# Kernel optimization log

Hardware: AMD Instinct MI355X
Metric: run time of the kernel (lower is better)

Reference implementation:

```python
import jax, jax.numpy as jnp
import numpy as np

# module config
D = 1024      # d_model
H = 16        # n_heads
DK = D // H   # head dim (rotary dim)
HI = 4        # indexer heads
DI = 64       # indexer dim
K = 512       # layer_top_k (adaptive_k fixed to layer default)
B, S = 2, 2048


def setup_inputs() -> dict:
    key = jax.random.key(0)
    ks = jax.random.split(key, 6)
    sc = 0.02
    return {
        "x": jax.random.normal(ks[0], (B, S, D), jnp.float32),
        "w_qkv": jax.random.normal(ks[1], (3 * D, D), jnp.float32) * sc,
        "w_o": jax.random.normal(ks[2], (D, D), jnp.float32) * sc,
        "w_qi": jax.random.normal(ks[3], (HI * DI, D), jnp.float32) * sc,
        "w_ki": jax.random.normal(ks[4], (DI, D), jnp.float32) * sc,
        "w_wi": jax.random.normal(ks[5], (HI, D), jnp.float32) * sc,
    }


def _rope(x):
    # torchtune-style interleaved RoPE; x: [b, s, h, d]
    d = x.shape[-1]
    s = x.shape[1]
    inv = 1.0 / (10000.0 ** (jnp.arange(0, d, 2, dtype=jnp.float32) / d))
    ang = jnp.arange(s, dtype=jnp.float32)[:, None] * inv  # [s, d/2]
    cos = jnp.cos(ang)[None, :, None, :]
    sin = jnp.sin(ang)[None, :, None, :]
    x1, x2 = x[..., ::2], x[..., 1::2]
    return jnp.stack([x1 * cos - x2 * sin, x1 * sin + x2 * cos], axis=-1).reshape(x.shape)


def reference(x, w_qkv, w_o, w_qi, w_ki, w_wi):
    b, s, _ = x.shape
    # QKV projection -> [b, s, 3, H, DK]
    qkv = (x @ w_qkv.T).reshape(b, s, 3, H, DK)
    q, k, v = qkv[:, :, 0], qkv[:, :, 1], qkv[:, :, 2]  # [b, s, h, dk]
    q = _rope(q)
    k = _rope(k)

    # Lightning indexer: I[t,s] = sum_j w[t,j] * relu(q_idx[t,j] . k_idx[s])
    qi = (x @ w_qi.T).reshape(b, s, HI, DI)
    ki = x @ w_ki.T            # [b, s, DI]
    wi = x @ w_wi.T            # [b, s, HI]
    dots = jnp.einsum('bthd,bsd->bths', qi, ki)
    idx_scores = (jax.nn.relu(dots) * wi[:, :, :, None]).sum(axis=2)  # [b, t, s]

    # causal mask then top-k selection -> boolean allow-mask via scatter
    causal = jnp.triu(jnp.ones((s, s), dtype=bool), 1)
    masked_scores = jnp.where(causal[None], -jnp.inf, idx_scores)
    _, top_idx = jax.lax.top_k(masked_scores, K)  # [b, t, K]
    allow = jnp.zeros((b, s, s), dtype=bool).at[
        jnp.arange(b)[:, None, None], jnp.arange(s)[None, :, None], top_idx
    ].set(True)

    # gated sparse attention: SDPA with additive mask (0 where selected, -inf else)
    scores = jnp.einsum('bthd,bshd->bhts', q, k) / jnp.sqrt(jnp.float32(DK))
    scores = jnp.where(allow[:, None], scores, -jnp.inf)
    attn = jax.nn.softmax(scores, axis=-1)
    out = jnp.einsum('bhts,bshd->bthd', attn, v).reshape(b, s, D)
    return out @ w_o.T
```

## Files before the change

### kernel.cpp

```cpp
#include <hip/hip_runtime.h>
#include <hip/hip_bf16.h>
#include <math.h>

namespace {

constexpr int cB = 2, cS = 2048, cD = 1024, cH = 16, cHI = 4, cDI = 64, cK = 512;
constexpr int cNT = cB * cS;
constexpr int QKV_STRIDE = 3 * cD;

typedef __bf16 bf16x8 __attribute__((ext_vector_type(8)));
typedef float f32x4 __attribute__((ext_vector_type(4)));

__device__ __forceinline__ unsigned packbf2(float a, float b)
{
    __hip_bfloat16 ba = __float2bfloat16(a), bb = __float2bfloat16(b);
    return (unsigned)*(unsigned short*)&ba | ((unsigned)*(unsigned short*)&bb << 16);
}

__global__ void pack_bf16(const float* __restrict__ src, __hip_bfloat16* __restrict__ dst, int n)
{
    int i = blockIdx.x * 256 + threadIdx.x;
    if (i < n) dst[i] = __float2bfloat16(src[i]);
}

__global__ __launch_bounds__(256) void mfma_gemm_bt(const __hip_bfloat16* __restrict__ A,
                                                    const __hip_bfloat16* __restrict__ B,
                                                    float* __restrict__ C, int M, int N, int K)
{
    __shared__ unsigned short Als[128][40];
    __shared__ unsigned short Bls[128][40];
    const int tid = threadIdx.x;
    const int m0 = blockIdx.y * 128, n0 = blockIdx.x * 128;
    const int w = tid >> 6, lane = tid & 63;
    const int mw = (w >> 1) * 64, nw = (w & 1) * 64;
    const int lr = lane & 15, quad = lane >> 4;
    const unsigned short* Au = (const unsigned short*)A;
    const unsigned short* Bu = (const unsigned short*)B;
    f32x4 acc[4][4] = {};
    for (int k0 = 0; k0 < K; k0 += 32) {
#pragma unroll
        for (int i = 0; i < 2; i++) {
            int c = tid + i * 256;
            int row = c >> 2, kc = c & 3;
            uint4 av = *(const uint4*)(Au + (size_t)(m0 + row) * K + k0 + kc * 8);
            uint4 bv = *(const uint4*)(Bu + (size_t)(n0 + row) * K + k0 + kc * 8);
            *(uint4*)&Als[row][kc * 8] = av;
            *(uint4*)&Bls[row][kc * 8] = bv;
        }
        __syncthreads();
        bf16x8 af[4], bfr[4];
#pragma unroll
        for (int i = 0; i < 4; i++) af[i] = *(const bf16x8*)&Als[mw + i * 16 + lr][quad * 8];
#pragma unroll
        for (int j = 0; j < 4; j++) bfr[j] = *(const bf16x8*)&Bls[nw + j * 16 + lr][quad * 8];
#pragma unroll
        for (int i = 0; i < 4; i++)
#pragma unroll
            for (int j = 0; j < 4; j++)
                acc[i][j] = __builtin_amdgcn_mfma_f32_16x16x32_bf16(af[i], bfr[j], acc[i][j], 0, 0, 0);
        __syncthreads();
    }
#pragma unroll
    for (int i = 0; i < 4; i++)
#pragma unroll
        for (int j = 0; j < 4; j++)
#pragma unroll
            for (int r = 0; r < 4; r++) {
                int m = m0 + mw + i * 16 + quad * 4 + r;
                int n = n0 + nw + j * 16 + lr;
                C[(size_t)m * N + n] = acc[i][j][r];
            }
}

__global__ __launch_bounds__(256) void gemm_idx(const float* __restrict__ A, const float* __restrict__ w_qi,
                                                const float* __restrict__ w_ki, const float* __restrict__ w_wi,
                                                float* __restrict__ qi, float* __restrict__ ki, float* __restrict__ wi)
{
    __shared__ float As[2][32][68];
    __shared__ float Bs[2][32][68];
    const int tid = threadIdx.x;
    const int m0 = blockIdx.y * 64, n0 = blockIdx.x * 64;
    const int ty = tid >> 4, tx = tid & 15;
    const int r = tid >> 5, kk = tid & 31;
    float aR[8], bR[8];

    auto loadStage = [&](int k0) {
#pragma unroll
        for (int i = 0; i < 8; i++) {
            aR[i] = A[(size_t)(m0 + r + i * 8) * cD + k0 + kk];
            const int nr = n0 + r + i * 8;
            float bv = 0.f;
            if (nr < 256) bv = w_qi[(size_t)nr * cD + k0 + kk];
            else if (nr < 320) bv = w_ki[(size_t)(nr - 256) * cD + k0 + kk];
            else if (nr < 324) bv = w_wi[(size_t)(nr - 320) * cD + k0 + kk];
            bR[i] = bv;
        }
    };
    auto commitStage = [&](int bf) {
#pragma unroll
        for (int i = 0; i < 8; i++) {
            As[bf][kk][r + i * 8] = aR[i];
            Bs[bf][kk][r + i * 8] = bR[i];
        }
    };

    loadStage(0);
    commitStage(0);
    __syncthreads();
    float acc[4][4] = {};
    for (int s = 0; s < 32; s++) {
        const int cb = s & 1;
        if (s < 31) loadStage((s + 1) * 32);
#pragma unroll
        for (int kx = 0; kx < 32; kx++) {
            float a[4], b[4];
#pragma unroll
            for (int i = 0; i < 4; i++) a[i] = As[cb][kx][ty * 4 + i];
#pragma unroll
            for (int j = 0; j < 4; j++) b[j] = Bs[cb][kx][tx * 4 + j];
#pragma unroll
            for (int i = 0; i < 4; i++)
#pragma unroll
                for (int j = 0; j < 4; j++) acc[i][j] = fmaf(a[i], b[j], acc[i][j]);
        }
        if (s < 31) {
            commitStage(cb ^ 1);
            __syncthreads();
        }
    }
#pragma unroll
    for (int i = 0; i < 4; i++) {
        int m = m0 + ty * 4 + i;
#pragma unroll
        for (int j = 0; j < 4; j++) {
            int n = n0 + tx * 4 + j;
            if (n < 256) qi[(size_t)m * 256 + n] = acc[i][j];
            else if (n < 320) ki[(size_t)m * 64 + (n - 256)] = acc[i][j];
            else if (n < 324) wi[(size_t)m * 4 + (n - 320)] = acc[i][j];
        }
    }
}

__global__ void rope_pack(const float* __restrict__ qkv, __hip_bfloat16* __restrict__ qkvb)
{
    const int idx = blockIdx.x * 256 + threadIdx.x;
    const int c = idx & 511, tok = idx >> 9;
    const int i = c & 31;
    const int s = tok & (cS - 1);
    const float inv = powf(10000.f, -(float)(2 * i) / 64.f);
    float sn, cs;
    sincosf((float)s * inv, &sn, &cs);
    const size_t base = (size_t)tok * QKV_STRIDE + (c >> 5) * 64 + 2 * i;
    unsigned* dst = (unsigned*)qkvb;
    float x1 = qkv[base], x2 = qkv[base + 1];
    dst[base >> 1] = packbf2(x1 * cs - x2 * sn, x1 * sn + x2 * cs);
    x1 = qkv[base + cD]; x2 = qkv[base + cD + 1];
    dst[(base + cD) >> 1] = packbf2(x1 * cs - x2 * sn, x1 * sn + x2 * cs);
    dst[(base + 2 * cD) >> 1] = packbf2(qkv[base + 2 * cD], qkv[base + 2 * cD + 1]);
}

__global__ __launch_bounds__(256) void indexer_scores(const float* __restrict__ qi,
                                                      const float* __restrict__ ki,
                                                      const float* __restrict__ wi,
                                                      float* __restrict__ scores)
{
    const int b = blockIdx.z;
    const int t0 = blockIdx.y * 128, s0 = blockIdx.x * 64;
    if (s0 > t0 + 127) return;
    __shared__ float Qs[128][68];
    __shared__ float Ks[64][68];
    const int tid = threadIdx.x;
    const int ty = tid >> 4, tx = tid & 15;
#pragma unroll
    for (int i = 0; i < 4; i++) {
        int c = tid + i * 256;
        int r = c >> 4, cq = c & 15;
        *(float4*)&Ks[r][cq * 4] = *(const float4*)&ki[((size_t)(b * cS + s0 + r)) * cDI + cq * 4];
    }
    float acc[8][4] = {};
    for (int h = 0; h < cHI; h++) {
        __syncthreads();
#pragma unroll
        for (int i = 0; i < 8; i++) {
            int c = tid + i * 256;
            int r = c >> 4, cq = c & 15;
            *(float4*)&Qs[r][cq * 4] =
                *(const float4*)&qi[((size_t)(b * cS + t0 + r)) * (cHI * cDI) + h * cDI + cq * 4];
        }
        __syncthreads();
        float w8[8];
#pragma unroll
        for (int i = 0; i < 8; i++) w8[i] = wi[((size_t)(b * cS + t0 + ty + i * 16)) * cHI + h];
        float dot[8][4] = {};
        for (int d = 0; d < 64; d += 4) {
            float4 a4[8], b4[4];
#pragma unroll
            for (int i = 0; i < 8; i++) a4[i] = *(const float4*)&Qs[ty + i * 16][d];
#pragma unroll
            for (int j = 0; j < 4; j++) b4[j] = *(const float4*)&Ks[tx + j * 16][d];
#pragma unroll
            for (int i = 0; i < 8; i++)
#pragma unroll
                for (int j = 0; j < 4; j++) {
                    dot[i][j] = fmaf(a4[i].x, b4[j].x, dot[i][j]);
                    dot[i][j] = fmaf(a4[i].y, b4[j].y, dot[i][j]);
                    dot[i][j] = fmaf(a4[i].z, b4[j].z, dot[i][j]);
                    dot[i][j] = fmaf(a4[i].w, b4[j].w, dot[i][j]);
                }
        }
#pragma unroll
        for (int i = 0; i < 8; i++)
#pragma unroll
            for (int j = 0; j < 4; j++) acc[i][j] += fmaxf(dot[i][j], 0.f) * w8[i];
    }
#pragma unroll
    for (int i = 0; i < 8; i++) {
        int t = t0 + ty + i * 16;
#pragma unroll
        for (int j = 0; j < 4; j++) {
            int s = s0 + tx + j * 16;
            if (s <= t) scores[((size_t)(b * cS) + t) * cS + s] = acc[i][j];
        }
    }
}

__device__ __forceinline__ unsigned mapf(float f)
{
    unsigned u = __float_as_uint(f);
    if (u == 0x80000000u) u = 0u;
    return (u & 0x80000000u) ? ~u : (u | 0x80000000u);
}

__global__ void topk_select(const float* __restrict__ scores, unsigned* __restrict__ allow_w)
{
    const int row = blockIdx.x;
    const int t = row & (cS - 1);
    const int tid = threadIdx.x;
    unsigned* aw = allow_w + (size_t)row * 64;
    if (t < cK) {
        if (tid < 64) aw[tid] = (tid < 16) ? 0xFFFFFFFFu : 0u;
        return;
    }
    const float* sr = scores + (size_t)row * cS;
    const int n = t + 1;
    __shared__ unsigned ukeys[cS];
    __shared__ int whist[4][16];
    __shared__ unsigned abits[64];
    __shared__ int wsum[4];
    __shared__ unsigned sh_prefix;
    __shared__ int sh_rem, sh_eqbase;
    for (int s = tid; s < n; s += 256) ukeys[s] = mapf(sr[s]);
    if (tid < 64) abits[tid] = 0u;
    if (tid == 0) { sh_prefix = 0u; sh_rem = cK; }
    __syncthreads();
    const int wl = tid >> 6, ln = tid & 63;
    for (int pass = 0; pass < 8; pass++) {
        const int shift = 28 - 4 * pass;
        const unsigned prefix = sh_prefix;
        const unsigned himask = pass ? (0xFFFFFFFFu << (shift + 4)) : 0u;
        unsigned cnt = 0;
        for (int sb = wl * 64; sb < n; sb += 256) {
            const int s = sb + ln;
            const bool active = (s < n) && ((ukeys[s] & himask) == prefix);
            const unsigned d = active ? ((ukeys[s] >> shift) & 15u) : 0u;
            const unsigned long long bA = __ballot(active);
            const unsigned long long b0 = __ballot((d & 1u) != 0u);
            const unsigned long long b1 = __ballot((d & 2u) != 0u);
            const unsigned long long b2 = __ballot((d & 4u) != 0u);
            const unsigned long long b3 = __ballot((d & 8u) != 0u);
            if (ln < 16) {
                unsigned long long mres = bA;
                mres &= (ln & 1) ? b0 : ~b0;
                mres &= (ln & 2) ? b1 : ~b1;
                mres &= (ln & 4) ? b2 : ~b2;
                mres &= (ln & 8) ? b3 : ~b3;
                cnt += (unsigned)__popcll(mres);
            }
        }
        if (ln < 16) whist[wl][ln] = (int)cnt;
        __syncthreads();
        if (tid == 0) {
            int rem = sh_rem, cum = 0, d = 15;
            for (; d > 0; d--) {
                const int hd = whist[0][d] + whist[1][d] + whist[2][d] + whist[3][d];
                if (cum + hd >= rem) break;
                cum += hd;
            }
            sh_prefix = prefix | ((unsigned)d << shift);
            sh_rem = rem - cum;
        }
        __syncthreads();
    }
    const unsigned Tu = sh_prefix;
    const int needEq = sh_rem;
    if (tid == 0) sh_eqbase = 0;
    __syncthreads();
    for (int s0 = 0; s0 < n; s0 += 256) {
        const int s = s0 + tid;
        const bool valid = s < n;
        const unsigned u = valid ? ukeys[s] : 0u;
        const bool gt = valid && (u > Tu);
        const bool eq = valid && (u == Tu);
        const unsigned long long bal = __ballot(eq);
        if (ln == 0) wsum[wl] = __popcll(bal);
        __syncthreads();
        int wpre = 0;
        for (int q = 0; q < wl; q++) wpre += wsum[q];
        const int eq_exc = sh_eqbase + wpre + __popcll(bal & ((1ull << ln) - 1ull));
        if (gt || (eq && eq_exc < needEq))
            atomicOr(&abits[s >> 5], 1u << (s & 31));
        const int eq_tot = wsum[0] + wsum[1] + wsum[2] + wsum[3];
        __syncthreads();
        if (tid == 0) sh_eqbase += eq_tot;
        __syncthreads();
    }
    if (tid < 64) aw[tid] = abits[tid];
}

__global__ void union_mask(const unsigned* __restrict__ allow_w, unsigned* __restrict__ umask_any)
{
    const int bt = blockIdx.x;
    const int wd = threadIdx.x;
    const unsigned* base = allow_w + (size_t)bt * 64 * 64 + wd;
    unsigned u = 0;
    for (int rr = 0; rr < 64; rr++) u |= base[rr * 64];
    const unsigned long long bal = __ballot(u != 0u);
    if (wd == 0) {
        unsigned any = 0;
        for (int kt = 0; kt < 32; kt++)
            if ((bal >> (2 * kt)) & 3ull) any |= 1u << kt;
        umask_any[bt] = any;
    }
}

__global__ __launch_bounds__(256) void flash_attn(const __hip_bfloat16* __restrict__ qkvb,
                                                  const unsigned* __restrict__ allow_w,
                                                  const unsigned* __restrict__ umask_any,
                                                  __hip_bfloat16* __restrict__ ao)
{
    __shared__ unsigned short Kls[2][64][76];
    __shared__ unsigned short Vt[2][64][74];
    __shared__ unsigned short Pls[4][16][74];
    __shared__ uint2 mask_l[2][64];
    const int ttile = 31 - blockIdx.x;
    const int h = blockIdx.y;
    const int b = blockIdx.z;
    const int tid = threadIdx.x;
    const int w = tid >> 6, lane = tid & 63;
    const int lr = lane & 15, quad = lane >> 4;
    const int tok0 = b * cS + ttile * 64;
    const unsigned short* qkvu = (const unsigned short*)qkvb;

    bf16x8 aq[2];
    {
        const size_t qoff = (size_t)(tok0 + w * 16 + lr) * QKV_STRIDE + h * 64 + quad * 8;
        aq[0] = *(const bf16x8*)(qkvu + qoff);
        aq[1] = *(const bf16x8*)(qkvu + qoff + 32);
    }

    f32x4 O[4] = {};
    float m_r[4], l_r[4];
#pragma unroll
    for (int r = 0; r < 4; r++) { m_r[r] = -INFINITY; l_r[r] = 0.f; }

    const int ktmax = (ttile > 7) ? ttile : 7;
    unsigned todo = umask_any[b * 32 + ttile];
    todo &= (ktmax == 31) ? 0xFFFFFFFFu : ((1u << (ktmax + 1)) - 1u);

    uint4 kreg[2], vreg[2];
    uint2 mreg = {0u, 0u};
    auto issue = [&](int kt) {
#pragma unroll
        for (int i = 0; i < 2; i++) {
            const int idx = tid + i * 256;
            const int key = idx >> 3, dg = idx & 7;
            const size_t base = (size_t)(b * cS + kt * 64 + key) * QKV_STRIDE + h * 64 + dg * 8;
            kreg[i] = *(const uint4*)(qkvu + cD + base);
            vreg[i] = *(const uint4*)(qkvu + 2 * cD + base);
        }
        if (tid < 64) mreg = *(const uint2*)&allow_w[(size_t)(tok0 + tid) * 64 + kt * 2];
    };
    auto commit = [&](int bf) {
#pragma unroll
        for (int i = 0; i < 2; i++) {
            const int idx = tid + i * 256;
            const int key = idx >> 3, dg = idx & 7;
            *(uint4*)&Kls[bf][key][dg * 8] = kreg[i];
            const unsigned short* vs = (const unsigned short*)&vreg[i];
#pragma unroll
            for (int jj = 0; jj < 8; jj++) Vt[bf][dg * 8 + jj][key] = vs[jj];
        }
        if (tid < 64) mask_l[bf][tid] = mreg;
    };

    issue(__ffs(todo) - 1);
    todo &= todo - 1;
    commit(0);
    __syncthreads();
    int buf = 0;
    for (;;) {
        const int ktn = todo ? (__ffs(todo) - 1) : -1;
        if (ktn >= 0) { todo &= todo - 1; issue(ktn); }

        f32x4 S[4];
#pragma unroll
        for (int j = 0; j < 4; j++) {
            bf16x8 bk0 = *(const bf16x8*)&Kls[buf][j * 16 + lr][quad * 8];
            bf16x8 bk1 = *(const bf16x8*)&Kls[buf][j * 16 + lr][32 + quad * 8];
            f32x4 s = {};
            s = __builtin_amdgcn_mfma_f32_16x16x32_bf16(aq[0], bk0, s, 0, 0, 0);
            s = __builtin_amdgcn_mfma_f32_16x16x32_bf16(aq[1], bk1, s, 0, 0, 0);
            S[j] = s;
        }
        uint2 mrow[4];
#pragma unroll
        for (int r = 0; r < 4; r++) mrow[r] = mask_l[buf][w * 16 + quad * 4 + r];
#pragma unroll
        for (int j = 0; j < 4; j++) {
            const int sh = (j & 1) * 16 + lr;
#pragma unroll
            for (int r = 0; r < 4; r++) {
                const unsigned mw = (j < 2) ? mrow[r].x : mrow[r].y;
                S[j][r] = ((mw >> sh) & 1u) ? S[j][r] * 0.125f : -INFINITY;
            }
        }
        float alpha[4], mu[4];
#pragma unroll
        for (int r = 0; r < 4; r++) {
            float tm = fmaxf(fmaxf(S[0][r], S[1][r]), fmaxf(S[2][r], S[3][r]));
#pragma unroll
            for (int msk = 8; msk; msk >>= 1) tm = fmaxf(tm, __shfl_xor(tm, msk));
            const float mnew = fmaxf(m_r[r], tm);
            const float mu_old = fmaxf(m_r[r], -1e30f);
            mu[r] = fmaxf(mnew, -1e30f);
            alpha[r] = __expf(mu_old - mu[r]);
            m_r[r] = mnew;
        }
        float rs[4] = {};
#pragma unroll
        for (int j = 0; j < 4; j++) {
#pragma unroll
            for (int r = 0; r < 4; r++) {
                const float p = __expf(S[j][r] - mu[r]);
                rs[r] += p;
                const __hip_bfloat16 pb = __float2bfloat16(p);
                Pls[w][quad * 4 + r][j * 16 + lr] = *(const unsigned short*)&pb;
            }
        }
#pragma unroll
        for (int r = 0; r < 4; r++) {
            float s = rs[r];
#pragma unroll
            for (int msk = 8; msk; msk >>= 1) s += __shfl_xor(s, msk);
            l_r[r] = l_r[r] * alpha[r] + s;
#pragma unroll
            for (int j = 0; j < 4; j++) O[j][r] *= alpha[r];
        }
        __syncthreads();

        bf16x8 ap0 = *(const bf16x8*)&Pls[w][lr][quad * 8];
        bf16x8 ap1 = *(const bf16x8*)&Pls[w][lr][32 + quad * 8];
#pragma unroll
        for (int j = 0; j < 4; j++) {
            bf16x8 bv0 = *(const bf16x8*)&Vt[buf][j * 16 + lr][quad * 8];
            bf16x8 bv1 = *(const bf16x8*)&Vt[buf][j * 16 + lr][32 + quad * 8];
            O[j] = __builtin_amdgcn_mfma_f32_16x16x32_bf16(ap0, bv0, O[j], 0, 0, 0);
            O[j] = __builtin_amdgcn_mfma_f32_16x16x32_bf16(ap1, bv1, O[j], 0, 0, 0);
        }
        if (ktn < 0) break;
        commit(buf ^ 1);
        __syncthreads();
        buf ^= 1;
    }

#pragma unroll
    for (int r = 0; r < 4; r++) {
        const float linv = 1.f / l_r[r];
        const size_t orow = (size_t)(tok0 + w * 16 + quad * 4 + r) * cD + h * 64;
#pragma unroll
        for (int j = 0; j < 4; j++)
            ao[orow + j * 16 + lr] = __float2bfloat16(O[j][r] * linv);
    }
}

}

extern "C" void kernel_launch(void* const* d_in, const int* in_sizes, int n_in,
                              void* d_out, int out_size, void* d_ws, size_t ws_size,
                              hipStream_t stream)
{
    const float* x     = (const float*)d_in[0];
    const float* w_qkv = (const float*)d_in[1];
    const float* w_o   = (const float*)d_in[2];
    const float* w_qi  = (const float*)d_in[3];
    const float* w_ki  = (const float*)d_in[4];
    const float* w_wi  = (const float*)d_in[5];
    float* out = (float*)d_out;

    float* qkv    = (float*)d_ws;
    float* qi     = qkv + (size_t)cNT * QKV_STRIDE;
    float* ki     = qi + (size_t)cNT * cHI * cDI;
    float* wi     = ki + (size_t)cNT * cDI;
    float* scores = wi + (size_t)cNT * cHI;
    unsigned* allow_w   = (unsigned*)(scores + (size_t)cB * cS * cS);
    __hip_bfloat16* wo_bf = (__hip_bfloat16*)(allow_w + (size_t)cNT * 64);
    unsigned* umask_any = (unsigned*)(wo_bf + (size_t)cD * cD);

    __hip_bfloat16* x_bf    = (__hip_bfloat16*)scores;
    __hip_bfloat16* wqkv_bf = x_bf + (size_t)cNT * cD;
    __hip_bfloat16* ao_bf  = (__hip_bfloat16*)scores;
    __hip_bfloat16* qkv_bf = ao_bf + (size_t)cNT * cD;

    pack_bf16<<<cNT * cD / 256, 256, 0, stream>>>(x, x_bf, cNT * cD);
    pack_bf16<<<3 * cD * cD / 256, 256, 0, stream>>>(w_qkv, wqkv_bf, 3 * cD * cD);
    mfma_gemm_bt<<<dim3(3 * cD / 128, cNT / 128), 256, 0, stream>>>(x_bf, wqkv_bf, qkv, cNT, 3 * cD, cD);
    gemm_idx<<<dim3(6, cNT / 64), 256, 0, stream>>>(x, w_qi, w_ki, w_wi, qi, ki, wi);
    indexer_scores<<<dim3(cS / 64, cS / 128, cB), 256, 0, stream>>>(qi, ki, wi, scores);
    topk_select<<<cNT, 256, 0, stream>>>(scores, allow_w);
    union_mask<<<cB * 32, 64, 0, stream>>>(allow_w, umask_any);
    rope_pack<<<cNT * 512 / 256, 256, 0, stream>>>(qkv, qkv_bf);
    pack_bf16<<<cD * cD / 256, 256, 0, stream>>>(w_o, wo_bf, cD * cD);
    flash_attn<<<dim3(cS / 64, cH, cB), 256, 0, stream>>>(qkv_bf, allow_w, umask_any, ao_bf);
    mfma_gemm_bt<<<dim3(cD / 128, cNT / 128), 256, 0, stream>>>(ao_bf, wo_bf, out, cNT, cD, cD);
}
```

Baseline: 604.5 us.

## Drop online-softmax max tracking and union-mask skip in sparse flash attention

Removes the running-max online softmax and exponentiates raw scaled scores directly, summing the denominator once at the end. This drops per-tile max reductions, the alpha rescaling and one barrier. It also removes the union_mask kernel and tile skipping, so every causal key tile up to ktmax is visited, and it replaces double-buffered LDS with a single buffer plus an extra sync. V is transposed with packed 32-bit LDS writes. Skipping max subtraction risks overflow if scores are large, and losing tile skipping adds work for tiles with no selected keys.

```diff
diff --git a/kernel.cpp b/kernel.cpp
--- a/kernel.cpp
+++ b/kernel.cpp
@@ -317,31 +317,14 @@
     if (tid < 64) aw[tid] = abits[tid];
 }
 
-__global__ void union_mask(const unsigned* __restrict__ allow_w, unsigned* __restrict__ umask_any)
-{
-    const int bt = blockIdx.x;
-    const int wd = threadIdx.x;
-    const unsigned* base = allow_w + (size_t)bt * 64 * 64 + wd;
-    unsigned u = 0;
-    for (int rr = 0; rr < 64; rr++) u |= base[rr * 64];
-    const unsigned long long bal = __ballot(u != 0u);
-    if (wd == 0) {
-        unsigned any = 0;
-        for (int kt = 0; kt < 32; kt++)
-            if ((bal >> (2 * kt)) & 3ull) any |= 1u << kt;
-        umask_any[bt] = any;
-    }
-}
-
 __global__ __launch_bounds__(256) void flash_attn(const __hip_bfloat16* __restrict__ qkvb,
                                                   const unsigned* __restrict__ allow_w,
-                                                  const unsigned* __restrict__ umask_any,
                                                   __hip_bfloat16* __restrict__ ao)
 {
-    __shared__ unsigned short Kls[2][64][76];
-    __shared__ unsigned short Vt[2][64][74];
-    __shared__ unsigned short Pls[4][16][74];
-    __shared__ uint2 mask_l[2][64];
+    __shared__ unsigned short Kls[64][72];
+    __shared__ unsigned short Vt[64][72];
+    __shared__ unsigned short Pls[4][16][72];
+    __shared__ uint2 mask_l[64];
     const int ttile = 31 - blockIdx.x;
     const int h = blockIdx.y;
     const int b = blockIdx.z;
@@ -359,123 +342,89 @@
     }
 
     f32x4 O[4] = {};
-    float m_r[4], l_r[4];
-#pragma unroll
-    for (int r = 0; r < 4; r++) { m_r[r] = -INFINITY; l_r[r] = 0.f; }
-
+    float l_acc[4] = {};
     const int ktmax = (ttile > 7) ? ttile : 7;
-    unsigned todo = umask_any[b * 32 + ttile];
-    todo &= (ktmax == 31) ? 0xFFFFFFFFu : ((1u << (ktmax + 1)) - 1u);
-
+
+    const int kkey = tid >> 3, kdg = tid & 7;
+    const int vkey2 = tid & 31, vdg = tid >> 5;
     uint4 kreg[2], vreg[2];
     uint2 mreg = {0u, 0u};
     auto issue = [&](int kt) {
-#pragma unroll
-        for (int i = 0; i < 2; i++) {
-            const int idx = tid + i * 256;
-            const int key = idx >> 3, dg = idx & 7;
-            const size_t base = (size_t)(b * cS + kt * 64 + key) * QKV_STRIDE + h * 64 + dg * 8;
-            kreg[i] = *(const uint4*)(qkvu + cD + base);
-            vreg[i] = *(const uint4*)(qkvu + 2 * cD + base);
-        }
+        const size_t krow = (size_t)(b * cS + kt * 64 + kkey) * QKV_STRIDE + cD + h * 64 + kdg * 8;
+        kreg[0] = *(const uint4*)(qkvu + krow);
+        kreg[1] = *(const uint4*)(qkvu + krow + 32 * QKV_STRIDE);
+        const size_t vrow = (size_t)(b * cS + kt * 64 + 2 * vkey2) * QKV_STRIDE + 2 * cD + h * 64 + vdg * 8;
+        vreg[0] = *(const uint4*)(qkvu + vrow);
+        vreg[1] = *(const uint4*)(qkvu + vrow + QKV_STRIDE);
         if (tid < 64) mreg = *(const uint2*)&allow_w[(size_t)(tok0 + tid) * 64 + kt * 2];
     };
-    auto commit = [&](int bf) {
-#pragma unroll
-        for (int i = 0; i < 2; i++) {
-            const int idx = tid + i * 256;
-            const int key = idx >> 3, dg = idx & 7;
-            *(uint4*)&Kls[bf][key][dg * 8] = kreg[i];
-            const unsigned short* vs = (const unsigned short*)&vreg[i];
-#pragma unroll
-            for (int jj = 0; jj < 8; jj++) Vt[bf][dg * 8 + jj][key] = vs[jj];
-        }
-        if (tid < 64) mask_l[bf][tid] = mreg;
+    auto commit = [&]() {
+        *(uint4*)&Kls[kkey][kdg * 8] = kreg[0];
+        *(uint4*)&Kls[kkey + 32][kdg * 8] = kreg[1];
+        const unsigned short* v0 = (const unsigned short*)&vreg[0];
+        const unsigned short* v1 = (const unsigned short*)&vreg[1];
+#pragma unroll
+        for (int jj = 0; jj < 8; jj++)
+            *(unsigned*)&Vt[vdg * 8 + jj][2 * vkey2] = (unsigned)v0[jj] | ((unsigned)v1[jj] << 16);
+        if (tid < 64) mask_l[tid] = mreg;
     };
 
-    issue(__ffs(todo) - 1);
-    todo &= todo - 1;
-    commit(0);
+    issue(0);
+    commit();
     __syncthreads();
-    int buf = 0;
-    for (;;) {
-        const int ktn = todo ? (__ffs(todo) - 1) : -1;
-        if (ktn >= 0) { todo &= todo - 1; issue(ktn); }
+    for (int kt = 0;;) {
+        const bool more = kt < ktmax;
+        if (more) issue(kt + 1);
 
         f32x4 S[4];
 #pragma unroll
         for (int j = 0; j < 4; j++) {
-            bf16x8 bk0 = *(const bf16x8*)&Kls[buf][j * 16 + lr][quad * 8];
-            bf16x8 bk1 = *(const bf16x8*)&Kls[buf][j * 16 + lr][32 + quad * 8];
+            bf16x8 bk0 = *(const bf16x8*)&Kls[j * 16 + lr][quad * 8];
+            bf16x8 bk1 = *(const bf16x8*)&Kls[j * 16 + lr][32 + quad * 8];
             f32x4 s = {};
             s = __builtin_amdgcn_mfma_f32_16x16x32_bf16(aq[0], bk0, s, 0, 0, 0);
             s = __builtin_amdgcn_mfma_f32_16x16x32_bf16(aq[1], bk1, s, 0, 0, 0);
             S[j] = s;
         }
+
         uint2 mrow[4];
 #pragma unroll
-        for (int r = 0; r < 4; r++) mrow[r] = mask_l[buf][w * 16 + quad * 4 + r];
+        for (int r = 0; r < 4; r++) mrow[r] = mask_l[w * 16 + quad * 4 + r];
 #pragma unroll
         for (int j = 0; j < 4; j++) {
             const int sh = (j & 1) * 16 + lr;
 #pragma unroll
             for (int r = 0; r < 4; r++) {
                 const unsigned mw = (j < 2) ? mrow[r].x : mrow[r].y;
-                S[j][r] = ((mw >> sh) & 1u) ? S[j][r] * 0.125f : -INFINITY;
-            }
-        }
-        float alpha[4], mu[4];
-#pragma unroll
-        for (int r = 0; r < 4; r++) {
-            float tm = fmaxf(fmaxf(S[0][r], S[1][r]), fmaxf(S[2][r], S[3][r]));
-#pragma unroll
-            for (int msk = 8; msk; msk >>= 1) tm = fmaxf(tm, __shfl_xor(tm, msk));
-            const float mnew = fmaxf(m_r[r], tm);
-            const float mu_old = fmaxf(m_r[r], -1e30f);
-            mu[r] = fmaxf(mnew, -1e30f);
-            alpha[r] = __expf(mu_old - mu[r]);
-            m_r[r] = mnew;
-        }
-        float rs[4] = {};
-#pragma unroll
-        for (int j = 0; j < 4; j++) {
-#pragma unroll
-            for (int r = 0; r < 4; r++) {
-                const float p = __expf(S[j][r] - mu[r]);
-                rs[r] += p;
+                const float p = ((mw >> sh) & 1u) ? __expf(S[j][r] * 0.125f) : 0.f;
+                l_acc[r] += p;
                 const __hip_bfloat16 pb = __float2bfloat16(p);
                 Pls[w][quad * 4 + r][j * 16 + lr] = *(const unsigned short*)&pb;
             }
         }
-#pragma unroll
-        for (int r = 0; r < 4; r++) {
-            float s = rs[r];
-#pragma unroll
-            for (int msk = 8; msk; msk >>= 1) s += __shfl_xor(s, msk);
-            l_r[r] = l_r[r] * alpha[r] + s;
-#pragma unroll
-            for (int j = 0; j < 4; j++) O[j][r] *= alpha[r];
-        }
-        __syncthreads();
 
         bf16x8 ap0 = *(const bf16x8*)&Pls[w][lr][quad * 8];
         bf16x8 ap1 = *(const bf16x8*)&Pls[w][lr][32 + quad * 8];
 #pragma unroll
         for (int j = 0; j < 4; j++) {
-            bf16x8 bv0 = *(const bf16x8*)&Vt[buf][j * 16 + lr][quad * 8];
-            bf16x8 bv1 = *(const bf16x8*)&Vt[buf][j * 16 + lr][32 + quad * 8];
+            bf16x8 bv0 = *(const bf16x8*)&Vt[j * 16 + lr][quad * 8];
+            bf16x8 bv1 = *(const bf16x8*)&Vt[j * 16 + lr][32 + quad * 8];
             O[j] = __builtin_amdgcn_mfma_f32_16x16x32_bf16(ap0, bv0, O[j], 0, 0, 0);
             O[j] = __builtin_amdgcn_mfma_f32_16x16x32_bf16(ap1, bv1, O[j], 0, 0, 0);
         }
-        if (ktn < 0) break;
-        commit(buf ^ 1);
-        __syncthreads();
-        buf ^= 1;
+        if (!more) break;
+        __syncthreads();
+        commit();
+        __syncthreads();
+        kt++;
     }
 
 #pragma unroll
     for (int r = 0; r < 4; r++) {
-        const float linv = 1.f / l_r[r];
+        float s = l_acc[r];
+#pragma unroll
+        for (int msk = 8; msk; msk >>= 1) s += __shfl_xor(s, msk);
+        const float linv = 1.f / s;
         const size_t orow = (size_t)(tok0 + w * 16 + quad * 4 + r) * cD + h * 64;
 #pragma unroll
         for (int j = 0; j < 4; j++)
@@ -504,7 +453,6 @@
     float* scores = wi + (size_t)cNT * cHI;
     unsigned* allow_w   = (unsigned*)(scores + (size_t)cB * cS * cS);
     __hip_bfloat16* wo_bf = (__hip_bfloat16*)(allow_w + (size_t)cNT * 64);
-    unsigned* umask_any = (unsigned*)(wo_bf + (size_t)cD * cD);
 
     __hip_bfloat16* x_bf    = (__hip_bfloat16*)scores;
     __hip_bfloat16* wqkv_bf = x_bf + (size_t)cNT * cD;
@@ -517,9 +465,8 @@
     gemm_idx<<<dim3(6, cNT / 64), 256, 0, stream>>>(x, w_qi, w_ki, w_wi, qi, ki, wi);
     indexer_scores<<<dim3(cS / 64, cS / 128, cB), 256, 0, stream>>>(qi, ki, wi, scores);
     topk_select<<<cNT, 256, 0, stream>>>(scores, allow_w);
-    union_mask<<<cB * 32, 64, 0, stream>>>(allow_w, umask_any);
     rope_pack<<<cNT * 512 / 256, 256, 0, stream>>>(qkv, qkv_bf);
     pack_bf16<<<cD * cD / 256, 256, 0, stream>>>(w_o, wo_bf, cD * cD);
-    flash_attn<<<dim3(cS / 64, cH, cB), 256, 0, stream>>>(qkv_bf, allow_w, umask_any, ao_bf);
+    flash_attn<<<dim3(cS / 64, cH, cB), 256, 0, stream>>>(qkv_bf, allow_w, ao_bf);
     mfma_gemm_bt<<<dim3(cD / 128, cNT / 128), 256, 0, stream>>>(ao_bf, wo_bf, out, cNT, cD, cD);
 }
```

Measured after the change: 544.3 us. 10.0% less time.
